# Kernel tuning notes

Hardware: AMD Instinct MI355X
Metric: run time of the kernel (lower is better)

The kernel has to match this reference:

```python
import math
import jax, jax.numpy as jnp
import numpy as np

DIM, NHEAD, TOPK = 1024, 16, 64
DK = DIM // NHEAD
HIDDEN = int(DIM * 8.0)
EPS = 1e-5


def setup_inputs() -> dict:
    key = jax.random.key(0)
    ks = jax.random.split(key, 12)
    B, T = 2, 2048
    s = 0.02
    return {
        "x": jax.random.normal(ks[0], (B, T, DIM), jnp.float32),
        "ln1_g": jnp.ones((DIM,), jnp.float32),
        "ln1_b": jnp.zeros((DIM,), jnp.float32),
        "w_qkv": jax.random.normal(ks[1], (DIM, 3 * DIM), jnp.float32) * s,
        "alpha_head": jnp.zeros((NHEAD,), jnp.float32),
        "w_out": jax.random.normal(ks[2], (DIM, DIM), jnp.float32) * s,
        "ln2_g": jnp.ones((DIM,), jnp.float32),
        "ln2_b": jnp.zeros((DIM,), jnp.float32),
        "w1": jax.random.normal(ks[3], (DIM, HIDDEN), jnp.float32) * s,
        "b1": jnp.zeros((HIDDEN,), jnp.float32),
        "w2": jax.random.normal(ks[4], (HIDDEN, DIM), jnp.float32) * s,
        "b2": jnp.zeros((DIM,), jnp.float32),
        "alpha": jnp.float32(0.5),
    }


def _layernorm(x, g, b):
    mu = jnp.mean(x, axis=-1, keepdims=True)
    var = jnp.var(x, axis=-1, keepdims=True)
    return (x - mu) * jax.lax.rsqrt(var + EPS) * g + b


def _adaptive_sparse_attn(xn, w_qkv, alpha_head, w_out):
    B, T, C = xn.shape
    qkv = xn @ w_qkv  # [B,T,3C]
    q, k, v = jnp.split(qkv, 3, axis=-1)
    def heads(t):
        return t.reshape(B, T, NHEAD, DK).transpose(0, 2, 1, 3)  # [B,H,T,dk]
    q, k, v = heads(q), heads(k), heads(v)
    attn = jnp.einsum("bhqd,bhkd->bhqk", q, k) / math.sqrt(DK)  # [B,H,T,T]
    dense = jnp.einsum("bhqk,bhkd->bhqd", jax.nn.softmax(attn, axis=-1), v)
    # top-k sparse branch (TOPK < T)
    _, idx = jax.lax.top_k(attn, TOPK)  # [B,H,T,TOPK]
    M = B * NHEAD * T
    keep = jnp.zeros((M, T), bool).at[jnp.arange(M)[:, None], idx.reshape(M, TOPK)].set(True)
    keep = keep.reshape(B, NHEAD, T, T)
    attn_sp = jnp.where(keep, attn, jnp.float32(-1e9))
    sparse = jnp.einsum("bhqk,bhkd->bhqd", jax.nn.softmax(attn_sp, axis=-1), v)
    gate = jax.nn.sigmoid(alpha_head)[None, :, None, None]
    out = gate * dense + (1.0 - gate) * sparse  # [B,H,T,dk]
    out = out.transpose(0, 2, 1, 3).reshape(B, T, C)
    return out @ w_out


def reference(x, ln1_g, ln1_b, w_qkv, alpha_head, w_out, ln2_g, ln2_b, w1, b1, w2, b2, alpha):
    # attention sub-block with learned residual scale alpha
    x = x + alpha * _adaptive_sparse_attn(_layernorm(x, ln1_g, ln1_b), w_qkv, alpha_head, w_out)
    # FFN (dropout in eval mode -> identity); exact GELU as torch default
    h = jax.nn.gelu(_layernorm(x, ln2_g, ln2_b) @ w1 + b1, approximate=False)
    x = x + alpha * (h @ w2 + b2)
    return x
```

## Files before the change

kernel.cpp:

```cpp
#include <hip/hip_runtime.h>
#include <hip/hip_bf16.h>
#include <math.h>

#define DIMC 1024
#define NHEADC 16
#define DKC 64
#define HIDC 8192
#define TSEQ 2048
#define BATCH 2
#define NROWS (BATCH*TSEQ)
#define EPSF 1e-5f

typedef __attribute__((ext_vector_type(8))) short short8;
typedef __attribute__((ext_vector_type(4))) float floatx4;

__device__ __forceinline__ unsigned pk2bf(float a, float b){
  float2 t; t.x = a; t.y = b;
  __hip_bfloat162 h = __float22bfloat162_rn(t);
  union { __hip_bfloat162 h; unsigned u; } cv; cv.h = h;
  return cv.u;
}
__device__ __forceinline__ ushort f2bf(float f){
  return (ushort)(pk2bf(f, f) & 0xFFFFu);
}
__device__ __forceinline__ floatx4 mfma16(short8 a, short8 b, floatx4 c){
  return __builtin_amdgcn_mfma_f32_16x16x32_bf16(a, b, c, 0, 0, 0);
}
__device__ __forceinline__ void gld_lds16(const void* g, void* l){
  __builtin_amdgcn_global_load_lds((const __attribute__((address_space(1))) unsigned*)g,
                                   (__attribute__((address_space(3))) unsigned*)l, 16, 0, 0);
}
__device__ __forceinline__ float wred_add(float v){
  #pragma unroll
  for (int o = 32; o > 0; o >>= 1) v += __shfl_xor(v, o, 64);
  return v;
}
__device__ __forceinline__ float wred_max(float v){
  #pragma unroll
  for (int o = 32; o > 0; o >>= 1) v = fmaxf(v, __shfl_xor(v, o, 64));
  return v;
}

__global__ __launch_bounds__(256)
void wconv_t(const float* __restrict__ W, ushort* __restrict__ WT, int K, int N)
{
  __shared__ float tile[32][33];
  const int t = threadIdx.x, tx = t & 31, ty = t >> 5;
  const int n0 = blockIdx.x * 32, k0 = blockIdx.y * 32;
  #pragma unroll
  for (int r = 0; r < 4; ++r)
    tile[ty + r*8][tx] = W[(size_t)(k0 + ty + r*8) * N + n0 + tx];
  __syncthreads();
  #pragma unroll
  for (int r = 0; r < 4; ++r)
    WT[(size_t)(n0 + ty + r*8) * K + k0 + tx] = f2bf(tile[tx][ty + r*8]);
}

__global__ __launch_bounds__(256)
void vtrans(const ushort* __restrict__ qkv, ushort* __restrict__ vT)
{
  const int d = threadIdx.x & 63, tp = threadIdx.x >> 6;
  const int bh = blockIdx.y; const int h = bh & 15, b = bh >> 4;
  const int t0 = blockIdx.x * 32 + tp * 8;
  const ushort* src = qkv + ((size_t)(b*TSEQ) + t0) * (3*DIMC) + 2*DIMC + h*DKC + d;
  ushort tmp[8];
  #pragma unroll
  for (int k = 0; k < 8; ++k) tmp[k] = src[(size_t)k * (3*DIMC)];
  *(short8*)&vT[((size_t)bh*DKC + d)*TSEQ + t0] = *(const short8*)tmp;
}

__global__ __launch_bounds__(256)
void ln_bf16(const float* __restrict__ x, const float* __restrict__ g,
             const float* __restrict__ b, ushort* __restrict__ y)
{
  __shared__ float red[8];
  const int row = blockIdx.x;
  const float* xr = x + (size_t)row * DIMC;
  const int c = threadIdx.x * 4;
  float4 v = *(const float4*)&xr[c];
  float s  = v.x + v.y + v.z + v.w;
  float ss = v.x*v.x + v.y*v.y + v.z*v.z + v.w*v.w;
  s = wred_add(s); ss = wred_add(ss);
  const int warp = threadIdx.x >> 6, lane = threadIdx.x & 63;
  if (lane == 0) { red[warp] = s; red[4+warp] = ss; }
  __syncthreads();
  s  = red[0] + red[1] + red[2] + red[3];
  ss = red[4] + red[5] + red[6] + red[7];
  const float mu  = s  * (1.f/DIMC);
  const float var = ss * (1.f/DIMC) - mu*mu;
  const float rr  = rsqrtf(var + EPSF);
  const float4 gv = *(const float4*)&g[c];
  const float4 bv = *(const float4*)&b[c];
  uint2 o;
  o.x = pk2bf((v.x-mu)*rr*gv.x + bv.x, (v.y-mu)*rr*gv.y + bv.y);
  o.y = pk2bf((v.z-mu)*rr*gv.z + bv.z, (v.w-mu)*rr*gv.w + bv.w);
  *(uint2*)&y[(size_t)row*DIMC + c] = o;
}

#define M_PLAIN 0
#define M_RES 1
#define M_BIAS_GELU 2
#define M_BIAS_RES 3

template<int MODE>
__global__ __launch_bounds__(256)
void gemm_bf16(const ushort* __restrict__ A, const ushort* __restrict__ BT,
               void* __restrict__ Cout, const int M, const int N, const int K,
               const float* __restrict__ bias, const float* __restrict__ res,
               const float* __restrict__ alphap)
{
  __shared__ __align__(16) ushort Al[4][128][8];
  __shared__ __align__(16) ushort Bl[4][128][8];
  const int t = threadIdx.x;
  const int lane = t & 63, warp = t >> 6;
  const int quad = lane >> 4, l16 = lane & 15;
  const int m0 = (warp & 1) * 64, n0 = (warp >> 1) * 64;
  const size_t row0 = (size_t)blockIdx.y * 128;
  const size_t col0 = (size_t)blockIdx.x * 128;

  const int c0 = t, c1 = t + 256;
  const int ar0 = c0 & 127, as0 = c0 >> 7;
  const int ar1 = c1 & 127, as1 = c1 >> 7;
  const ushort* pa0 = A  + (row0 + ar0) * (size_t)K + as0 * 8;
  const ushort* pa1 = A  + (row0 + ar1) * (size_t)K + as1 * 8;
  const ushort* pb0 = BT + (col0 + ar0) * (size_t)K + as0 * 8;
  const ushort* pb1 = BT + (col0 + ar1) * (size_t)K + as1 * 8;
  ushort* la0 = &Al[as0][ar0][0];
  ushort* la1 = &Al[as1][ar1][0];
  ushort* lb0 = &Bl[as0][ar0][0];
  ushort* lb1 = &Bl[as1][ar1][0];

  floatx4 acc[4][4];
  const floatx4 zf = {0.f, 0.f, 0.f, 0.f};
  #pragma unroll
  for (int i = 0; i < 4; ++i)
    #pragma unroll
    for (int j = 0; j < 4; ++j) acc[i][j] = zf;

  for (int k0 = 0; k0 < K; k0 += 32) {
    gld_lds16(pa0 + k0, la0);
    gld_lds16(pa1 + k0, la1);
    gld_lds16(pb0 + k0, lb0);
    gld_lds16(pb1 + k0, lb1);
    __syncthreads();
    short8 af[4], bfr[4];
    #pragma unroll
    for (int i = 0; i < 4; ++i) {
      af[i]  = *(const short8*)&Al[quad][m0 + i*16 + l16][0];
      bfr[i] = *(const short8*)&Bl[quad][n0 + i*16 + l16][0];
    }
    #pragma unroll
    for (int mt = 0; mt < 4; ++mt)
      #pragma unroll
      for (int nt = 0; nt < 4; ++nt)
        acc[mt][nt] = mfma16(af[mt], bfr[nt], acc[mt][nt]);
    __syncthreads();
  }

  float alpha = 0.f;
  if (MODE == M_RES || MODE == M_BIAS_RES) alpha = alphap[0];
  #pragma unroll
  for (int nt = 0; nt < 4; ++nt) {
    const size_t col = col0 + n0 + nt*16 + l16;
    float bv = 0.f;
    if (MODE == M_BIAS_GELU || MODE == M_BIAS_RES) bv = bias[col];
    #pragma unroll
    for (int mt = 0; mt < 4; ++mt) {
      const size_t r0 = row0 + m0 + mt*16 + quad*4;
      #pragma unroll
      for (int reg = 0; reg < 4; ++reg) {
        float v = acc[mt][nt][reg];
        if (MODE == M_BIAS_GELU || MODE == M_BIAS_RES) v += bv;
        if (MODE == M_BIAS_GELU) v = 0.5f*v*(1.f + erff(v*0.70710678118654752f));
        if (MODE == M_RES || MODE == M_BIAS_RES) v = res[(r0+reg)*(size_t)N + col] + alpha*v;
        if (MODE == M_PLAIN || MODE == M_BIAS_GELU)
          ((ushort*)Cout)[(r0+reg)*(size_t)N + col] = f2bf(v);
        else
          ((float*)Cout)[(r0+reg)*(size_t)N + col] = v;
      }
    }
  }
}

__device__ __forceinline__ int swzf(int q){ return ((q>>2) ^ q) & 7; }
__device__ __forceinline__ int sidx(int q, int j){
  return (q << 11) + ((((j >> 3) ^ swzf(q)) << 3) | (j & 7));
}

__global__ __launch_bounds__(1024, 8)
void attn_mfma(const ushort* __restrict__ qkv, const ushort* __restrict__ vT,
               const float* __restrict__ alpha_head, ushort* __restrict__ att)
{
  __shared__ __align__(16) ushort S[16*2048];
  __shared__ float Ored[3][4][16*17];
  const int t = threadIdx.x;
  const int lane = t & 63, warp = t >> 6;
  const int quad = lane >> 4, l16 = lane & 15;
  const int blk = blockIdx.x;
  const int bh  = blk >> 7;
  const int q0  = (blk & 127) << 4;
  const int h = bh & (NHEADC-1), b = bh >> 4;
  const size_t rowbase = (size_t)b * TSEQ;
  const floatx4 zf = {0.f, 0.f, 0.f, 0.f};

  {
    const ushort* Qp = qkv + (rowbase + q0 + l16) * (size_t)(3*DIMC) + h*DKC + quad*8;
    const short8 aq0 = *(const short8*)Qp;
    const short8 aq1 = *(const short8*)(Qp + 32);
    const int j0w = warp * 128;
    #pragma unroll
    for (int jt = 0; jt < 8; ++jt) {
      const int j = j0w + jt*16;
      const ushort* Kp = qkv + (rowbase + j + l16) * (size_t)(3*DIMC) + DIMC + h*DKC + quad*8;
      const short8 kb0 = *(const short8*)Kp;
      const short8 kb1 = *(const short8*)(Kp + 32);
      floatx4 c = mfma16(aq0, kb0, zf);
      c = mfma16(aq1, kb1, c);
      #pragma unroll
      for (int r = 0; r < 4; ++r)
        S[sidx(quad*4 + r, j + l16)] = f2bf(c[r]);
    }
  }
  __syncthreads();

  const float SC2 = 0.125f * 1.4426950408889634f;
  const float gate = 1.f / (1.f + __expf(-alpha_head[h]));
  {
    const int q = warp;
    const int sbase = q << 11;
    const int swq = swzf(q);
    float sv[32];
    float mx = -3.0e38f;
    #pragma unroll
    for (int p = 0; p < 16; ++p) {
      const int j = 2*lane + 128*p;
      const int g = (j >> 3) ^ swq;
      const unsigned pr = *(const unsigned*)&S[sbase + (g << 3) + (j & 7)];
      const float v0 = __uint_as_float(pr << 16);
      const float v1 = __uint_as_float(pr & 0xFFFF0000u);
      sv[2*p] = v0; sv[2*p+1] = v1;
      mx = fmaxf(mx, fmaxf(v0, v1));
    }
    mx = wred_max(mx);
    const float nc = -mx * SC2;

    unsigned prefix = 0u;
    for (int bit = 15; bit >= 0; --bit) {
      const unsigned cand = prefix | (1u << bit);
      const unsigned ub = (cand >= 0x8000u) ? (cand - 0x8000u) : (0xFFFFu - cand);
      const float candf = __uint_as_float(ub << 16);
      int c = 0;
      #pragma unroll
      for (int i = 0; i < 32; ++i)
        c += __popcll(__ballot(sv[i] >= candf));
      if (c >= 64) prefix = cand;
    }
    const unsigned ubf = (prefix >= 0x8000u) ? (prefix - 0x8000u) : (0xFFFFu - prefix);
    const float thf = __uint_as_float(ubf << 16);

    unsigned inmask = 0u;
    int c_gt = 0;
    #pragma unroll
    for (int i = 0; i < 32; ++i) {
      const bool gbit = sv[i] > thf;
      c_gt += __popcll(__ballot(gbit));
      if (gbit) inmask |= (1u << i);
    }
    const int need_eq = 64 - c_gt;
    int eqb = 0;
    const unsigned long long below = (1ULL << lane) - 1ULL;
    for (int p = 0; p < 16; ++p) {
      const bool e0 = (sv[2*p]   == thf);
      const bool e1 = (sv[2*p+1] == thf);
      const unsigned long long m0 = __ballot(e0);
      const unsigned long long m1 = __ballot(e1);
      if (m0 | m1) {
        const int r0 = eqb + __popcll(m0 & below) + __popcll(m1 & below);
        const int r1 = r0 + (e0 ? 1 : 0);
        if (e0 && r0 < need_eq) inmask |= (1u << (2*p));
        if (e1 && r1 < need_eq) inmask |= (1u << (2*p+1));
        eqb += __popcll(m0) + __popcll(m1);
      }
    }

    float sum_all = 0.f, sum_sp = 0.f;
    #pragma unroll
    for (int i = 0; i < 32; ++i) {
      const float e = exp2f(fmaf(sv[i], SC2, nc));
      sum_all += e;
      sum_sp  += ((inmask >> i) & 1u) ? e : 0.f;
    }
    sum_all = wred_add(sum_all);
    sum_sp  = wred_add(sum_sp);

    const float cd  = gate / sum_all;
    const float cdc = cd + (1.f - gate) / sum_sp;
    #pragma unroll
    for (int p = 0; p < 16; ++p) {
      const float e0 = exp2f(fmaf(sv[2*p],   SC2, nc));
      const float e1 = exp2f(fmaf(sv[2*p+1], SC2, nc));
      const float w0 = e0 * (((inmask >> (2*p))   & 1u) ? cdc : cd);
      const float w1 = e1 * (((inmask >> (2*p+1)) & 1u) ? cdc : cd);
      const int j = 2*lane + 128*p;
      const int g = (j >> 3) ^ swq;
      *(unsigned*)&S[sbase + (g << 3) + (j & 7)] = pk2bf(w0, w1);
    }
  }
  __syncthreads();

  const int ng = warp & 3, kq = warp >> 2;
  const int n0  = ng * 16;
  const int kt0 = kq * 16;
  floatx4 o = zf, o2 = zf;
  const ushort* Vb = vT + ((size_t)bh*DKC + n0 + l16) * TSEQ + quad*8;
  #pragma unroll 2
  for (int tt = 0; tt < 16; tt += 2) {
    const int kt = kt0 + tt;
    const short8 a0 = *(const short8*)&S[sidx(l16, kt*32 + quad*8)];
    const short8 vb0 = *(const short8*)(Vb + (size_t)kt*32);
    const short8 a1 = *(const short8*)&S[sidx(l16, (kt+1)*32 + quad*8)];
    const short8 vb1 = *(const short8*)(Vb + (size_t)(kt+1)*32);
    o  = mfma16(a0, vb0, o);
    o2 = mfma16(a1, vb1, o2);
  }
  o = o + o2;
  if (kq > 0) {
    #pragma unroll
    for (int r = 0; r < 4; ++r) Ored[kq-1][ng][(quad*4+r)*17 + l16] = o[r];
  }
  __syncthreads();
  if (kq == 0) {
    #pragma unroll
    for (int r = 0; r < 4; ++r) {
      const int ri = (quad*4+r)*17 + l16;
      const float v = o[r] + Ored[0][ng][ri] + Ored[1][ng][ri] + Ored[2][ng][ri];
      att[(rowbase + q0 + quad*4 + r) * (size_t)DIMC + h*DKC + n0 + l16] = f2bf(v);
    }
  }
}

extern "C" void kernel_launch(void* const* d_in, const int* in_sizes, int n_in,
                              void* d_out, int out_size, void* d_ws, size_t ws_size,
                              hipStream_t stream)
{
  const float* x          = (const float*)d_in[0];
  const float* ln1_g      = (const float*)d_in[1];
  const float* ln1_b      = (const float*)d_in[2];
  const float* w_qkv      = (const float*)d_in[3];
  const float* alpha_head = (const float*)d_in[4];
  const float* w_out      = (const float*)d_in[5];
  const float* ln2_g      = (const float*)d_in[6];
  const float* ln2_b      = (const float*)d_in[7];
  const float* w1         = (const float*)d_in[8];
  const float* b1         = (const float*)d_in[9];
  const float* w2         = (const float*)d_in[10];
  const float* b2         = (const float*)d_in[11];
  const float* alphap     = (const float*)d_in[12];
  float* out = (float*)d_out;

  char* ws = (char*)d_ws;
  ushort* wT_qkv = (ushort*)(ws);
  ushort* wT_out = (ushort*)(ws + 6291456);
  ushort* wT_1   = (ushort*)(ws + 8388608);
  ushort* wT_2   = (ushort*)(ws + 25165824);
  ushort* xn     = (ushort*)(ws + 41943040);
  ushort* qkv    = (ushort*)(ws + 50331648);
  ushort* attb   = (ushort*)(ws + 75497472);
  float*  x2     = (float*) (ws + 83886080);
  ushort* hbuf   = (ushort*)(ws + 100663296);
  ushort* vT     = (ushort*)(ws + 167772160);

  wconv_t<<<dim3(3072/32, 1024/32), 256, 0, stream>>>(w_qkv, wT_qkv, 1024, 3072);
  wconv_t<<<dim3(1024/32, 1024/32), 256, 0, stream>>>(w_out, wT_out, 1024, 1024);
  wconv_t<<<dim3(8192/32, 1024/32), 256, 0, stream>>>(w1,    wT_1,   1024, 8192);
  wconv_t<<<dim3(1024/32, 8192/32), 256, 0, stream>>>(w2,    wT_2,   8192, 1024);

  ln_bf16<<<NROWS, 256, 0, stream>>>(x, ln1_g, ln1_b, xn);
  gemm_bf16<M_PLAIN><<<dim3(3*DIMC/128, NROWS/128), 256, 0, stream>>>(
      xn, wT_qkv, qkv, NROWS, 3*DIMC, DIMC, nullptr, nullptr, nullptr);
  vtrans<<<dim3(64, 32), 256, 0, stream>>>(qkv, vT);
  attn_mfma<<<4096, 1024, 0, stream>>>(qkv, vT, alpha_head, attb);
  gemm_bf16<M_RES><<<dim3(DIMC/128, NROWS/128), 256, 0, stream>>>(
      attb, wT_out, x2, NROWS, DIMC, DIMC, nullptr, x, alphap);
  ln_bf16<<<NROWS, 256, 0, stream>>>(x2, ln2_g, ln2_b, xn);
  gemm_bf16<M_BIAS_GELU><<<dim3(HIDC/128, NROWS/128), 256, 0, stream>>>(
      xn, wT_1, hbuf, NROWS, HIDC, DIMC, b1, nullptr, nullptr);
  gemm_bf16<M_BIAS_RES><<<dim3(DIMC/128, NROWS/128), 256, 0, stream>>>(
      hbuf, wT_2, out, NROWS, DIMC, HIDC, b2, x2, alphap);
}
```

Baseline: 990.5 us.

## Deepen GEMM K-step to 64 and use integer keys in top-k select

The bf16 GEMM now loads a 64-wide K slice per iteration into doubled LDS buffers, which halves the number of barrier pairs per tile. The attention top-k radix search now compares precomputed monotone integer keys rather than converted floats, and the exponentials are computed once and cached instead of being recomputed in two passes. The attention kernel's launch-bounds occupancy hint drops from 8 to 4, giving the compiler room for the extra kk/ev register arrays. The costs are more LDS per GEMM block and more live registers in attention.

Result: slower. 1.164 ms (+17.5%).

```diff
diff --git a/kernel.cpp b/kernel.cpp
--- a/kernel.cpp
+++ b/kernel.cpp
@@ -35,10 +35,19 @@
   for (int o = 32; o > 0; o >>= 1) v += __shfl_xor(v, o, 64);
   return v;
 }
-__device__ __forceinline__ float wred_max(float v){
-  #pragma unroll
-  for (int o = 32; o > 0; o >>= 1) v = fmaxf(v, __shfl_xor(v, o, 64));
+__device__ __forceinline__ int wred_maxi(int v){
+  #pragma unroll
+  for (int o = 32; o > 0; o >>= 1) v = max(v, __shfl_xor(v, o, 64));
   return v;
+}
+__device__ __forceinline__ float lo16f(unsigned u){ return __uint_as_float(u << 16); }
+__device__ __forceinline__ float hi16f(unsigned u){ return __uint_as_float(u & 0xFFFF0000u); }
+__device__ __forceinline__ unsigned bfkey(unsigned u16v){
+  return (u16v & 0x8000u) ? ((~u16v) & 0xFFFFu) : (u16v | 0x8000u);
+}
+__device__ __forceinline__ float keyf(unsigned k){
+  const unsigned ub = (k >= 0x8000u) ? (k - 0x8000u) : (0xFFFFu - k);
+  return __uint_as_float(ub << 16);
 }
 
 __global__ __launch_bounds__(256)
@@ -109,8 +118,8 @@
                const float* __restrict__ bias, const float* __restrict__ res,
                const float* __restrict__ alphap)
 {
-  __shared__ __align__(16) ushort Al[4][128][8];
-  __shared__ __align__(16) ushort Bl[4][128][8];
+  __shared__ __align__(16) ushort Al[8][128][8];
+  __shared__ __align__(16) ushort Bl[8][128][8];
   const int t = threadIdx.x;
   const int lane = t & 63, warp = t >> 6;
   const int quad = lane >> 4, l16 = lane & 15;
@@ -118,17 +127,17 @@
   const size_t row0 = (size_t)blockIdx.y * 128;
   const size_t col0 = (size_t)blockIdx.x * 128;
 
-  const int c0 = t, c1 = t + 256;
-  const int ar0 = c0 & 127, as0 = c0 >> 7;
-  const int ar1 = c1 & 127, as1 = c1 >> 7;
-  const ushort* pa0 = A  + (row0 + ar0) * (size_t)K + as0 * 8;
-  const ushort* pa1 = A  + (row0 + ar1) * (size_t)K + as1 * 8;
-  const ushort* pb0 = BT + (col0 + ar0) * (size_t)K + as0 * 8;
-  const ushort* pb1 = BT + (col0 + ar1) * (size_t)K + as1 * 8;
-  ushort* la0 = &Al[as0][ar0][0];
-  ushort* la1 = &Al[as1][ar1][0];
-  ushort* lb0 = &Bl[as0][ar0][0];
-  ushort* lb1 = &Bl[as1][ar1][0];
+  const ushort* pa[4]; const ushort* pb[4];
+  ushort* la[4]; ushort* lb[4];
+  #pragma unroll
+  for (int i = 0; i < 4; ++i) {
+    const int idx = t + i*256;
+    const int ar = idx & 127, as = idx >> 7;
+    pa[i] = A  + (row0 + ar) * (size_t)K + as * 8;
+    pb[i] = BT + (col0 + ar) * (size_t)K + as * 8;
+    la[i] = &Al[as][ar][0];
+    lb[i] = &Bl[as][ar][0];
+  }
 
   floatx4 acc[4][4];
   const floatx4 zf = {0.f, 0.f, 0.f, 0.f};
@@ -137,23 +146,28 @@
     #pragma unroll
     for (int j = 0; j < 4; ++j) acc[i][j] = zf;
 
-  for (int k0 = 0; k0 < K; k0 += 32) {
-    gld_lds16(pa0 + k0, la0);
-    gld_lds16(pa1 + k0, la1);
-    gld_lds16(pb0 + k0, lb0);
-    gld_lds16(pb1 + k0, lb1);
+  for (int k0 = 0; k0 < K; k0 += 64) {
+    #pragma unroll
+    for (int i = 0; i < 4; ++i) {
+      gld_lds16(pa[i] + k0, la[i]);
+      gld_lds16(pb[i] + k0, lb[i]);
+    }
     __syncthreads();
-    short8 af[4], bfr[4];
-    #pragma unroll
-    for (int i = 0; i < 4; ++i) {
-      af[i]  = *(const short8*)&Al[quad][m0 + i*16 + l16][0];
-      bfr[i] = *(const short8*)&Bl[quad][n0 + i*16 + l16][0];
-    }
-    #pragma unroll
-    for (int mt = 0; mt < 4; ++mt)
-      #pragma unroll
-      for (int nt = 0; nt < 4; ++nt)
-        acc[mt][nt] = mfma16(af[mt], bfr[nt], acc[mt][nt]);
+    #pragma unroll
+    for (int half = 0; half < 2; ++half) {
+      const int ks = quad + half*4;
+      short8 af[4], bfr[4];
+      #pragma unroll
+      for (int i = 0; i < 4; ++i) {
+        af[i]  = *(const short8*)&Al[ks][m0 + i*16 + l16][0];
+        bfr[i] = *(const short8*)&Bl[ks][n0 + i*16 + l16][0];
+      }
+      #pragma unroll
+      for (int mt = 0; mt < 4; ++mt)
+        #pragma unroll
+        for (int nt = 0; nt < 4; ++nt)
+          acc[mt][nt] = mfma16(af[mt], bfr[nt], acc[mt][nt]);
+    }
     __syncthreads();
   }
 
@@ -187,7 +201,7 @@
   return (q << 11) + ((((j >> 3) ^ swzf(q)) << 3) | (j & 7));
 }
 
-__global__ __launch_bounds__(1024, 8)
+__global__ __launch_bounds__(1024, 4)
 void attn_mfma(const ushort* __restrict__ qkv, const ushort* __restrict__ vT,
                const float* __restrict__ alpha_head, ushort* __restrict__ att)
 {
@@ -229,40 +243,44 @@
     const int q = warp;
     const int sbase = q << 11;
     const int swq = swzf(q);
-    float sv[32];
-    float mx = -3.0e38f;
-    #pragma unroll
-    for (int p = 0; p < 16; ++p) {
-      const int j = 2*lane + 128*p;
-      const int g = (j >> 3) ^ swq;
-      const unsigned pr = *(const unsigned*)&S[sbase + (g << 3) + (j & 7)];
-      const float v0 = __uint_as_float(pr << 16);
-      const float v1 = __uint_as_float(pr & 0xFFFF0000u);
-      sv[2*p] = v0; sv[2*p+1] = v1;
-      mx = fmaxf(mx, fmaxf(v0, v1));
-    }
-    mx = wred_max(mx);
-    const float nc = -mx * SC2;
+    unsigned kk[32];
+    float ev[32];
+    int kmax = 0;
+    {
+      unsigned pk[16];
+      #pragma unroll
+      for (int p = 0; p < 16; ++p) {
+        const int j = 2*lane + 128*p;
+        const int g = (j >> 3) ^ swq;
+        pk[p] = *(const unsigned*)&S[sbase + (g << 3) + (j & 7)];
+        kk[2*p]   = bfkey(pk[p] & 0xFFFFu);
+        kk[2*p+1] = bfkey(pk[p] >> 16);
+        kmax = max(kmax, max((int)kk[2*p], (int)kk[2*p+1]));
+      }
+      kmax = wred_maxi(kmax);
+      const float nc = -keyf((unsigned)kmax) * SC2;
+      #pragma unroll
+      for (int p = 0; p < 16; ++p) {
+        ev[2*p]   = exp2f(fmaf(lo16f(pk[p]), SC2, nc));
+        ev[2*p+1] = exp2f(fmaf(hi16f(pk[p]), SC2, nc));
+      }
+    }
 
     unsigned prefix = 0u;
     for (int bit = 15; bit >= 0; --bit) {
       const unsigned cand = prefix | (1u << bit);
-      const unsigned ub = (cand >= 0x8000u) ? (cand - 0x8000u) : (0xFFFFu - cand);
-      const float candf = __uint_as_float(ub << 16);
       int c = 0;
       #pragma unroll
       for (int i = 0; i < 32; ++i)
-        c += __popcll(__ballot(sv[i] >= candf));
+        c += __popcll(__ballot(kk[i] >= cand));
       if (c >= 64) prefix = cand;
     }
-    const unsigned ubf = (prefix >= 0x8000u) ? (prefix - 0x8000u) : (0xFFFFu - prefix);
-    const float thf = __uint_as_float(ubf << 16);
 
     unsigned inmask = 0u;
     int c_gt = 0;
     #pragma unroll
     for (int i = 0; i < 32; ++i) {
-      const bool gbit = sv[i] > thf;
+      const bool gbit = kk[i] > prefix;
       c_gt += __popcll(__ballot(gbit));
       if (gbit) inmask |= (1u << i);
     }
@@ -270,8 +288,8 @@
     int eqb = 0;
     const unsigned long long below = (1ULL << lane) - 1ULL;
     for (int p = 0; p < 16; ++p) {
-      const bool e0 = (sv[2*p]   == thf);
-      const bool e1 = (sv[2*p+1] == thf);
+      const bool e0 = (kk[2*p]   == prefix);
+      const bool e1 = (kk[2*p+1] == prefix);
       const unsigned long long m0 = __ballot(e0);
       const unsigned long long m1 = __ballot(e1);
       if (m0 | m1) {
@@ -286,9 +304,8 @@
     float sum_all = 0.f, sum_sp = 0.f;
     #pragma unroll
     for (int i = 0; i < 32; ++i) {
-      const float e = exp2f(fmaf(sv[i], SC2, nc));
-      sum_all += e;
-      sum_sp  += ((inmask >> i) & 1u) ? e : 0.f;
+      sum_all += ev[i];
+      sum_sp  += ((inmask >> i) & 1u) ? ev[i] : 0.f;
     }
     sum_all = wred_add(sum_all);
     sum_sp  = wred_add(sum_sp);
@@ -297,10 +314,8 @@
     const float cdc = cd + (1.f - gate) / sum_sp;
     #pragma unroll
     for (int p = 0; p < 16; ++p) {
-      const float e0 = exp2f(fmaf(sv[2*p],   SC2, nc));
-      const float e1 = exp2f(fmaf(sv[2*p+1], SC2, nc));
-      const float w0 = e0 * (((inmask >> (2*p))   & 1u) ? cdc : cd);
-      const float w1 = e1 * (((inmask >> (2*p+1)) & 1u) ? cdc : cd);
+      const float w0 = ev[2*p]   * (((inmask >> (2*p))   & 1u) ? cdc : cd);
+      const float w1 = ev[2*p+1] * (((inmask >> (2*p+1)) & 1u) ? cdc : cd);
       const int j = 2*lane + 128*p;
       const int g = (j >> 3) ^ swq;
       *(unsigned*)&S[sbase + (g << 3) + (j & 7)] = pk2bf(w0, w1);
```
